# Optimization experiments

Measured on AMD Instinct MI355X. Metric: run time of the kernel, lower is better.

Reference implementation:

```python
import jax, jax.numpy as jnp
import numpy as np

IN_DIM = 4096
OUT_DIM = 4096
RANK = 64
MULTIPLIER = 1.0
SCALE = 1.0  # alpha / lora_dim = 64 / 64


def setup_inputs() -> dict:
    key = jax.random.key(0)
    ks = jax.random.split(key, 8)
    x = jax.random.normal(ks[0], (4, 4096, IN_DIM), dtype=jnp.float32)
    # frozen original module weight (Linear, no bias): [out, in]
    W_org = jax.random.normal(ks[1], (OUT_DIM, IN_DIM), dtype=jnp.float32) * 0.02
    # trainable adapter: q (down) [r, in], p (up) [out, r], lambda [1, r]
    q_w = jax.random.normal(ks[2], (RANK, IN_DIM), dtype=jnp.float32) * 0.02
    p_w = jax.random.normal(ks[3], (OUT_DIM, RANK), dtype=jnp.float32) * 0.02
    lam = jnp.abs(jax.random.normal(ks[4], (1, RANK), dtype=jnp.float32)) / np.sqrt(RANK)
    # frozen base copies (deepcopied at init; here distinct values to exercise the subtraction)
    base_q_w = jax.random.normal(ks[5], (RANK, IN_DIM), dtype=jnp.float32) * 0.02
    base_p_w = jax.random.normal(ks[6], (OUT_DIM, RANK), dtype=jnp.float32) * 0.02
    base_lam = jnp.abs(jax.random.normal(ks[7], (1, RANK), dtype=jnp.float32)) / np.sqrt(RANK)
    return {"x": x, "W_org": W_org, "q_w": q_w, "p_w": p_w, "lam": lam,
            "base_q_w": base_q_w, "base_p_w": base_p_w, "base_lam": base_lam}


def reference(x, W_org, q_w, p_w, lam, base_q_w, base_p_w, base_lam):
    # original module forward (Linear, no bias)
    org = jnp.einsum('bsd,od->bso', x, W_org)
    # adapter path: P((Q x) * lambda)
    lx = jnp.einsum('bsr,or->bso', jnp.einsum('bsd,rd->bsr', x, q_w) * lam, p_w)
    # frozen base path: base_P((base_Q x) * base_lambda)
    base_lx = jnp.einsum('bsr,or->bso', jnp.einsum('bsd,rd->bsr', x, base_q_w) * base_lam, base_p_w)
    return org + (lx - base_lx) * (MULTIPLIER * SCALE)
```

## Files before the change

kernel.cpp:

```cpp
#include <hip/hip_runtime.h>
#include <hip/hip_bf16.h>

typedef __hip_bfloat16 bf16;
typedef __attribute__((ext_vector_type(8))) short short8;
typedef __attribute__((ext_vector_type(4))) float floatx4;

#define K_DIM 4096
#define N_DIM 4096
#define M_DIM 16384
#define RANK  64

__global__ __launch_bounds__(256) void cvt_x_kernel(
    const float4* __restrict__ in, short8* __restrict__ out)
{
    const int i = blockIdx.x * 256 + threadIdx.x;
    const float4 a = in[2 * i];
    const float4 b = in[2 * i + 1];
    bf16 t[8];
    t[0] = __float2bfloat16(a.x); t[1] = __float2bfloat16(a.y);
    t[2] = __float2bfloat16(a.z); t[3] = __float2bfloat16(a.w);
    t[4] = __float2bfloat16(b.x); t[5] = __float2bfloat16(b.y);
    t[6] = __float2bfloat16(b.z); t[7] = __float2bfloat16(b.w);
    out[i] = *(const short8*)t;
}

__global__ __launch_bounds__(256) void prep_weff_kernel(
    const float* __restrict__ W, const float* __restrict__ q,
    const float* __restrict__ p, const float* __restrict__ lam,
    const float* __restrict__ bq, const float* __restrict__ bp,
    const float* __restrict__ blam, bf16* __restrict__ Weff)
{
    const int k  = blockIdx.x * 256 + threadIdx.x;
    const int n0 = blockIdx.y * 8;
    float acc[8];
#pragma unroll
    for (int i = 0; i < 8; ++i) acc[i] = 0.0f;

    for (int r = 0; r < RANK; ++r) {
        const float qlv  = lam[r]  * q [r * K_DIM + k];
        const float bqlv = blam[r] * bq[r * K_DIM + k];
#pragma unroll
        for (int i = 0; i < 8; ++i) {
            acc[i] += p [(n0 + i) * RANK + r] * qlv;
            acc[i] -= bp[(n0 + i) * RANK + r] * bqlv;
        }
    }
#pragma unroll
    for (int i = 0; i < 8; ++i) {
        const size_t idx = (size_t)(n0 + i) * K_DIM + k;
        Weff[idx] = __float2bfloat16(W[idx] + acc[i]);
    }
}

__device__ __forceinline__ void stage2(const bf16* g0, const bf16* g1, char* d)
{
    __builtin_amdgcn_global_load_lds(
        (const __attribute__((address_space(1))) void*)g0,
        (__attribute__((address_space(3))) void*)d, 16, 0, 0);
    __builtin_amdgcn_global_load_lds(
        (const __attribute__((address_space(1))) void*)g1,
        (__attribute__((address_space(3))) void*)(d + 8192), 16, 0, 0);
}

__device__ __forceinline__ void lda4(short8 (&dst)[4], const char* base,
                                     int off, int kb)
{
#pragma unroll
    for (int fr = 0; fr < 4; ++fr)
        dst[fr] = *(const short8*)(base + off + fr * 2048 + kb);
}

__device__ __forceinline__ void ldb4(short8 (&dst)[4], const char* base,
                                     int off, int kb)
{
#pragma unroll
    for (int fc = 0; fc < 4; ++fc)
        dst[fc] = *(const short8*)(base + off + fc * 2048 + kb);
}

__device__ __forceinline__ void mma16(floatx4 (&acc)[8][4], int rbase,
                                      const short8 (&av)[4], const short8 (&bv)[4])
{
#pragma unroll
    for (int fr = 0; fr < 4; ++fr)
#pragma unroll
        for (int fc = 0; fc < 4; ++fc)
            acc[rbase + fr][fc] = __builtin_amdgcn_mfma_f32_16x16x32_bf16(
                av[fr], bv[fc], acc[rbase + fr][fc], 0, 0, 0);
}

#define PHASE_TAIL(R0_, AV_, BV_) do {                         \
    __builtin_amdgcn_s_barrier();                              \
    asm volatile("s_waitcnt lgkmcnt(0)" ::: "memory");         \
    __builtin_amdgcn_s_setprio(1);                             \
    mma16(acc, R0_, AV_, BV_);                                 \
    __builtin_amdgcn_s_setprio(0);                             \
    __builtin_amdgcn_s_barrier();                              \
} while (0)

#define PHASE_TAIL_VM(R0_, AV_, BV_) do {                      \
    __builtin_amdgcn_s_barrier();                              \
    asm volatile("s_waitcnt lgkmcnt(0)" ::: "memory");         \
    __builtin_amdgcn_s_setprio(1);                             \
    mma16(acc, R0_, AV_, BV_);                                 \
    __builtin_amdgcn_s_setprio(0);                             \
    asm volatile("s_waitcnt vmcnt(4)" ::: "memory");           \
    __builtin_amdgcn_s_barrier();                              \
} while (0)

__global__ __launch_bounds__(512, 2) void gemm256_8ph_kernel(
    const bf16* __restrict__ A, const bf16* __restrict__ B, float* __restrict__ C)
{
    __shared__ __align__(16) char lds_buf[131072];

    const int tid  = threadIdx.x;
    const int lane = tid & 63;
    const int wave = tid >> 6;
    const int wm   = wave >> 2;
    const int wn   = wave & 3;

    const int bid = blockIdx.x;
    const int wg  = (bid & 7) * 128 + (bid >> 3);
    const int bx  = wg & 15;
    const int by  = wg >> 4;
    const int tm  = by * 256;
    const int tn  = bx * 256;

    const int r0  = tid >> 3;
    const int csw = (((tid & 7) ^ (r0 & 7)) << 3);
    const bf16* gA0 = A + (size_t)(tm +       r0) * K_DIM + csw;
    const bf16* gA1 = A + (size_t)(tm +  64 + r0) * K_DIM + csw;
    const bf16* gA2 = A + (size_t)(tm + 128 + r0) * K_DIM + csw;
    const bf16* gA3 = A + (size_t)(tm + 192 + r0) * K_DIM + csw;
    const bf16* gB0 = B + (size_t)(tn +       r0) * K_DIM + csw;
    const bf16* gB1 = B + (size_t)(tn +  64 + r0) * K_DIM + csw;
    const bf16* gB2 = B + (size_t)(tn + 128 + r0) * K_DIM + csw;
    const bf16* gB3 = B + (size_t)(tn + 192 + r0) * K_DIM + csw;

    char* ldsA = (char*)lds_buf;
    char* ldsB = ldsA + 32768;
    const int wb = wave * 1024;

    const int l15 = lane & 15;
    const int kb0 = ((lane >> 4) << 4) ^ ((lane & 7) << 4);
    const int kb1 = kb0 ^ 64;
    const char* aB = ldsA + (wm * 128 + l15) * 128;
    const char* bB = ldsB + (wn * 64  + l15) * 128;

    floatx4 acc[8][4];
#pragma unroll
    for (int p = 0; p < 8; ++p)
#pragma unroll
        for (int q = 0; q < 4; ++q) acc[p][q] = (floatx4){0.f, 0.f, 0.f, 0.f};

    short8 a0k0[4], a0k1[4], a1k0[4], a1k1[4], bk0[4], bk1[4];

    stage2(gA0, gA1, ldsA + wb);
    stage2(gA2, gA3, ldsA + 16384 + wb);
    stage2(gB0, gB1, ldsB + wb);
    stage2(gB2, gB3, ldsB + 16384 + wb);
    stage2(gA0 + 64, gA1 + 64, ldsA + 65536 + wb);
    stage2(gA2 + 64, gA3 + 64, ldsA + 65536 + 16384 + wb);
    asm volatile("s_waitcnt vmcnt(4)" ::: "memory");
    __builtin_amdgcn_s_barrier();

#pragma unroll 1
    for (int i = 0; i < 32; ++i) {
        const int kt1 = (2 * i + 1) * 64;
        const int kt2 = ((2 * i + 2 < 64) ? (2 * i + 2) : 63) * 64;
        const int kt3 = ((2 * i + 3 < 64) ? (2 * i + 3) : 63) * 64;

        lda4(a0k0, aB, 0, kb0);
        lda4(a0k1, aB, 0, kb1);
        ldb4(bk0, bB, 0, kb0);
        stage2(gB0 + kt1, gB1 + kt1, ldsB + 65536 + wb);
        PHASE_TAIL(0, a0k0, bk0);

        lda4(a1k0, aB, 8192, kb0);
        lda4(a1k1, aB, 8192, kb1);
        stage2(gB2 + kt1, gB3 + kt1, ldsB + 65536 + 16384 + wb);
        PHASE_TAIL(4, a1k0, bk0);

        ldb4(bk1, bB, 0, kb1);
        stage2(gA0 + kt2, gA1 + kt2, ldsA + wb);
        PHASE_TAIL(0, a0k1, bk1);

        stage2(gA2 + kt2, gA3 + kt2, ldsA + 16384 + wb);
        PHASE_TAIL_VM(4, a1k1, bk1);

        lda4(a0k0, aB, 65536, kb0);
        lda4(a0k1, aB, 65536, kb1);
        ldb4(bk0, bB, 65536, kb0);
        stage2(gB0 + kt2, gB1 + kt2, ldsB + wb);
        PHASE_TAIL(0, a0k0, bk0);

        lda4(a1k0, aB, 65536 + 8192, kb0);
        lda4(a1k1, aB, 65536 + 8192, kb1);
        stage2(gB2 + kt2, gB3 + kt2, ldsB + 16384 + wb);
        PHASE_TAIL(4, a1k0, bk0);

        ldb4(bk1, bB, 65536, kb1);
        stage2(gA0 + kt3, gA1 + kt3, ldsA + 65536 + wb);
        PHASE_TAIL(0, a0k1, bk1);

        stage2(gA2 + kt3, gA3 + kt3, ldsA + 65536 + 16384 + wb);
        PHASE_TAIL_VM(4, a1k1, bk1);
    }

    const int row0 = tm + wm * 128 + (lane >> 4) * 4;
    const int col0 = tn + wn * 64 + l15;
#pragma unroll
    for (int mf = 0; mf < 8; ++mf)
#pragma unroll
        for (int fc = 0; fc < 4; ++fc)
#pragma unroll
            for (int rr = 0; rr < 4; ++rr)
                C[(size_t)(row0 + mf * 16 + rr) * N_DIM + (col0 + fc * 16)] =
                    acc[mf][fc][rr];
}

extern "C" void kernel_launch(void* const* d_in, const int* in_sizes, int n_in,
                              void* d_out, int out_size, void* d_ws, size_t ws_size,
                              hipStream_t stream)
{
    const float* x    = (const float*)d_in[0];
    const float* Worg = (const float*)d_in[1];
    const float* qw   = (const float*)d_in[2];
    const float* pw   = (const float*)d_in[3];
    const float* lam  = (const float*)d_in[4];
    const float* bqw  = (const float*)d_in[5];
    const float* bpw  = (const float*)d_in[6];
    const float* blam = (const float*)d_in[7];
    float* out = (float*)d_out;

    bf16* x_bf = (bf16*)d_ws;
    bf16* Weff = (bf16*)((char*)d_ws + (size_t)M_DIM * K_DIM * 2);

    cvt_x_kernel<<<dim3((M_DIM * K_DIM) / (8 * 256)), 256, 0, stream>>>(
        (const float4*)x, (short8*)x_bf);

    prep_weff_kernel<<<dim3(K_DIM / 256, N_DIM / 8), 256, 0, stream>>>(
        Worg, qw, pw, lam, bqw, bpw, blam, Weff);

    gemm256_8ph_kernel<<<dim3(1024), 512, 0, stream>>>(x_bf, Weff, out);
}
```

Before: 1.058 ms.

## Triple-buffer B tiles in LDS and relax LDS waitcnt in GEMM phases

Enlarges LDS to 160KB so B tiles get a rotating three-buffer scheme, letting B loads for a k-tile be issued a full tile earlier than A. The prologue now preloads two k-tiles of both A and B. Some phases wait only until four LDS reads remain outstanding rather than all of them, so MFMAs can start on operands that have already arrived. The cost is higher LDS use per block, which with two blocks per CU may exceed LDS capacity and lower occupancy, plus more complex buffer-index bookkeeping.

```diff
diff --git a/kernel.cpp b/kernel.cpp
--- a/kernel.cpp
+++ b/kernel.cpp
@@ -89,29 +89,29 @@
                 av[fr], bv[fc], acc[rbase + fr][fc], 0, 0, 0);
 }
 
-#define PHASE_TAIL(R0_, AV_, BV_) do {                         \
+#define PHASE_TAIL(LG_, R0_, AV_, BV_) do {                    \
+    __builtin_amdgcn_s_barrier();                              \
+    asm volatile("s_waitcnt lgkmcnt(" #LG_ ")" ::: "memory");  \
+    __builtin_amdgcn_s_setprio(1);                             \
+    mma16(acc, R0_, AV_, BV_);                                 \
+    __builtin_amdgcn_s_setprio(0);                             \
+    __builtin_amdgcn_s_barrier();                              \
+} while (0)
+
+#define PHASE_TAIL_VM(R0_, AV_, BV_) do {                      \
     __builtin_amdgcn_s_barrier();                              \
     asm volatile("s_waitcnt lgkmcnt(0)" ::: "memory");         \
     __builtin_amdgcn_s_setprio(1);                             \
     mma16(acc, R0_, AV_, BV_);                                 \
     __builtin_amdgcn_s_setprio(0);                             \
-    __builtin_amdgcn_s_barrier();                              \
-} while (0)
-
-#define PHASE_TAIL_VM(R0_, AV_, BV_) do {                      \
-    __builtin_amdgcn_s_barrier();                              \
-    asm volatile("s_waitcnt lgkmcnt(0)" ::: "memory");         \
-    __builtin_amdgcn_s_setprio(1);                             \
-    mma16(acc, R0_, AV_, BV_);                                 \
-    __builtin_amdgcn_s_setprio(0);                             \
-    asm volatile("s_waitcnt vmcnt(4)" ::: "memory");           \
+    asm volatile("s_waitcnt vmcnt(8)" ::: "memory");           \
     __builtin_amdgcn_s_barrier();                              \
 } while (0)
 
 __global__ __launch_bounds__(512, 2) void gemm256_8ph_kernel(
     const bf16* __restrict__ A, const bf16* __restrict__ B, float* __restrict__ C)
 {
-    __shared__ __align__(16) char lds_buf[131072];
+    __shared__ __align__(16) char lds_buf[163840];
 
     const int tid  = threadIdx.x;
     const int lane = tid & 63;
@@ -138,7 +138,7 @@
     const bf16* gB3 = B + (size_t)(tn + 192 + r0) * K_DIM + csw;
 
     char* ldsA = (char*)lds_buf;
-    char* ldsB = ldsA + 32768;
+    char* ldsB = ldsA + 65536;
     const int wb = wave * 1024;
 
     const int l15 = lane & 15;
@@ -157,54 +157,59 @@
 
     stage2(gA0, gA1, ldsA + wb);
     stage2(gA2, gA3, ldsA + 16384 + wb);
+    stage2(gA0 + 64, gA1 + 64, ldsA + 32768 + wb);
+    stage2(gA2 + 64, gA3 + 64, ldsA + 32768 + 16384 + wb);
     stage2(gB0, gB1, ldsB + wb);
     stage2(gB2, gB3, ldsB + 16384 + wb);
-    stage2(gA0 + 64, gA1 + 64, ldsA + 65536 + wb);
-    stage2(gA2 + 64, gA3 + 64, ldsA + 65536 + 16384 + wb);
-    asm volatile("s_waitcnt vmcnt(4)" ::: "memory");
+    stage2(gB0 + 64, gB1 + 64, ldsB + 32768 + wb);
+    stage2(gB2 + 64, gB3 + 64, ldsB + 32768 + 16384 + wb);
+    asm volatile("s_waitcnt vmcnt(0)" ::: "memory");
     __builtin_amdgcn_s_barrier();
+
+    int bO0 = 0, bO1 = 32768, bO2 = 65536;
 
 #pragma unroll 1
     for (int i = 0; i < 32; ++i) {
-        const int kt1 = (2 * i + 1) * 64;
         const int kt2 = ((2 * i + 2 < 64) ? (2 * i + 2) : 63) * 64;
         const int kt3 = ((2 * i + 3 < 64) ? (2 * i + 3) : 63) * 64;
 
         lda4(a0k0, aB, 0, kb0);
+        ldb4(bk0, bB, bO0, kb0);
         lda4(a0k1, aB, 0, kb1);
-        ldb4(bk0, bB, 0, kb0);
-        stage2(gB0 + kt1, gB1 + kt1, ldsB + 65536 + wb);
-        PHASE_TAIL(0, a0k0, bk0);
+        stage2(gB0 + kt2, gB1 + kt2, ldsB + bO2 + wb);
+        PHASE_TAIL(4, 0, a0k0, bk0);
 
         lda4(a1k0, aB, 8192, kb0);
         lda4(a1k1, aB, 8192, kb1);
-        stage2(gB2 + kt1, gB3 + kt1, ldsB + 65536 + 16384 + wb);
-        PHASE_TAIL(4, a1k0, bk0);
-
-        ldb4(bk1, bB, 0, kb1);
+        stage2(gB2 + kt2, gB3 + kt2, ldsB + bO2 + 16384 + wb);
+        PHASE_TAIL(4, 4, a1k0, bk0);
+
+        ldb4(bk1, bB, bO0, kb1);
         stage2(gA0 + kt2, gA1 + kt2, ldsA + wb);
-        PHASE_TAIL(0, a0k1, bk1);
+        PHASE_TAIL(0, 0, a0k1, bk1);
 
         stage2(gA2 + kt2, gA3 + kt2, ldsA + 16384 + wb);
         PHASE_TAIL_VM(4, a1k1, bk1);
 
-        lda4(a0k0, aB, 65536, kb0);
-        lda4(a0k1, aB, 65536, kb1);
-        ldb4(bk0, bB, 65536, kb0);
-        stage2(gB0 + kt2, gB1 + kt2, ldsB + wb);
-        PHASE_TAIL(0, a0k0, bk0);
-
-        lda4(a1k0, aB, 65536 + 8192, kb0);
-        lda4(a1k1, aB, 65536 + 8192, kb1);
-        stage2(gB2 + kt2, gB3 + kt2, ldsB + 16384 + wb);
-        PHASE_TAIL(4, a1k0, bk0);
-
-        ldb4(bk1, bB, 65536, kb1);
-        stage2(gA0 + kt3, gA1 + kt3, ldsA + 65536 + wb);
-        PHASE_TAIL(0, a0k1, bk1);
-
-        stage2(gA2 + kt3, gA3 + kt3, ldsA + 65536 + 16384 + wb);
+        lda4(a0k0, aB, 32768, kb0);
+        ldb4(bk0, bB, bO1, kb0);
+        lda4(a0k1, aB, 32768, kb1);
+        stage2(gB0 + kt3, gB1 + kt3, ldsB + bO0 + wb);
+        PHASE_TAIL(4, 0, a0k0, bk0);
+
+        lda4(a1k0, aB, 32768 + 8192, kb0);
+        lda4(a1k1, aB, 32768 + 8192, kb1);
+        stage2(gB2 + kt3, gB3 + kt3, ldsB + bO0 + 16384 + wb);
+        PHASE_TAIL(4, 4, a1k0, bk0);
+
+        ldb4(bk1, bB, bO1, kb1);
+        stage2(gA0 + kt3, gA1 + kt3, ldsA + 32768 + wb);
+        PHASE_TAIL(0, 0, a0k1, bk1);
+
+        stage2(gA2 + kt3, gA3 + kt3, ldsA + 32768 + 16384 + wb);
         PHASE_TAIL_VM(4, a1k1, bk1);
+
+        const int tmp = bO2; bO2 = bO1; bO1 = bO0; bO0 = tmp;
     }
 
     const int row0 = tm + wm * 128 + (lane >> 4) * 4;
```

Result: no change. 1.053 ms (-0.5%).
